# Kernel optimization log

Measured on AMD Instinct MI355X. Metric: run time of the kernel, lower is better.

## Reference

```python
import jax, jax.numpy as jnp
import numpy as np
from jax import lax

D_MODEL = 192
D_STATE = 16
D_CONV = 4
EXPAND = 2
D_INNER = D_MODEL * EXPAND           # 384
DT_RANK = (D_MODEL + 15) // 16       # 12
B, H, W = 4, 32, 32
N = H * W                            # 1024


def layernorm(x, g, b, eps=1e-5):
    m = x.mean(-1, keepdims=True)
    v = ((x - m) ** 2).mean(-1, keepdims=True)
    return (x - m) / jnp.sqrt(v + eps) * g + b


def mamba(u, Win, cw, cb, Wxp, Wdt, bdt, Alog, Dp, Wout):
    """mamba-ssm Mamba block. u: (B, L, d_model)."""
    Bb, L, _ = u.shape
    xz = u @ Win.T                                  # (B,L,2*d_inner)
    xh, z = jnp.split(xz, 2, axis=-1)
    # causal depthwise conv1d
    xc = xh.transpose(0, 2, 1)                      # (B,d_inner,L)
    xc = lax.conv_general_dilated(
        xc, cw[:, None, :], (1,), [(D_CONV - 1, 0)],
        feature_group_count=D_INNER,
        dimension_numbers=('NCH', 'OIH', 'NCH')) + cb[None, :, None]
    xs = jax.nn.silu(xc).transpose(0, 2, 1)         # (B,L,d_inner)
    dbl = xs @ Wxp.T                                # (B,L,dt_rank+2*d_state)
    dt = dbl[..., :DT_RANK]
    Bm = dbl[..., DT_RANK:DT_RANK + D_STATE]
    Cm = dbl[..., DT_RANK + D_STATE:]
    dt = jax.nn.softplus(dt @ Wdt.T + bdt)          # (B,L,d_inner)
    A = -jnp.exp(Alog)                              # (d_inner,d_state)

    def step(h, inp):
        dt_t, B_t, C_t, x_t = inp                   # (B,di),(B,ds),(B,ds),(B,di)
        dA = jnp.exp(dt_t[..., None] * A)           # (B,di,ds)
        h = dA * h + dt_t[..., None] * B_t[:, None, :] * x_t[..., None]
        return h, jnp.einsum('bds,bs->bd', h, C_t)

    h0 = jnp.zeros((Bb, D_INNER, D_STATE), u.dtype)
    _, ys = lax.scan(step, h0, (dt.transpose(1, 0, 2), Bm.transpose(1, 0, 2),
                                Cm.transpose(1, 0, 2), xs.transpose(1, 0, 2)))
    y = ys.transpose(1, 0, 2) + xs * Dp
    y = y * jax.nn.silu(z)
    return y @ Wout.T


mamba4 = jax.vmap(mamba)  # batched over the 4 scan directions


def to_col(x):    # row-major -> column-major sequence order
    return x.reshape(-1, H, W, D_MODEL).transpose(0, 2, 1, 3).reshape(-1, N, D_MODEL)


def from_col(x):  # inverse of to_col
    return x.reshape(-1, W, H, D_MODEL).transpose(0, 2, 1, 3).reshape(-1, N, D_MODEL)


def setup_inputs() -> dict:
    key = jax.random.key(0)
    ks = iter(jax.random.split(key, 32))
    s = 0.02
    d, di, ds, r = D_MODEL, D_INNER, D_STATE, DT_RANK
    inp = {}
    inp['x'] = jax.random.normal(next(ks), (B, d, H, W), jnp.float32)
    inp['norm_g'] = jnp.ones((d,), jnp.float32)
    inp['norm_b'] = jnp.zeros((d,), jnp.float32)
    inp['in_w'] = jax.random.normal(next(ks), (d, d), jnp.float32) * s
    inp['in_b'] = jnp.zeros((d,), jnp.float32)
    # 4 stacked Mamba blocks
    inp['m_in_w'] = jax.random.normal(next(ks), (4, 2 * di, d), jnp.float32) * s
    inp['m_conv_w'] = jax.random.normal(next(ks), (4, di, D_CONV), jnp.float32) * s
    inp['m_conv_b'] = jnp.zeros((4, di), jnp.float32)
    inp['m_xp_w'] = jax.random.normal(next(ks), (4, r + 2 * ds, di), jnp.float32) * s
    inp['m_dt_w'] = jax.random.normal(next(ks), (4, di, r), jnp.float32) * s
    inp['m_dt_b'] = jax.random.normal(next(ks), (4, di), jnp.float32) * 0.1 - 4.0
    inp['m_Alog'] = jnp.log(jnp.tile(jnp.arange(1, ds + 1, dtype=jnp.float32), (4, di, 1)))
    inp['m_D'] = jnp.ones((4, di), jnp.float32)
    inp['m_out_w'] = jax.random.normal(next(ks), (4, d, di), jnp.float32) * s
    # fusion MLP
    inp['f_w1'] = jax.random.normal(next(ks), (2 * d, 4 * d), jnp.float32) * s
    inp['f_b1'] = jnp.zeros((2 * d,), jnp.float32)
    inp['f_w2'] = jax.random.normal(next(ks), (d, 2 * d), jnp.float32) * s
    inp['f_b2'] = jnp.zeros((d,), jnp.float32)
    inp['o_w'] = jax.random.normal(next(ks), (d, d), jnp.float32) * s
    inp['o_b'] = jnp.zeros((d,), jnp.float32)
    inp['on_g'] = jnp.ones((d,), jnp.float32)
    inp['on_b'] = jnp.zeros((d,), jnp.float32)
    return inp


def reference(x, norm_g, norm_b, in_w, in_b, m_in_w, m_conv_w, m_conv_b,
              m_xp_w, m_dt_w, m_dt_b, m_Alog, m_D, m_out_w,
              f_w1, f_b1, f_w2, f_b2, o_w, o_b, on_g, on_b):
    xs = x.reshape(B, D_MODEL, N).transpose(0, 2, 1)     # b c h w -> b (hw) c
    xs = layernorm(xs, norm_g, norm_b)
    xp = xs @ in_w.T + in_b
    col = to_col(xp)
    seqs = jnp.stack([xp, jnp.flip(xp, 1), col, jnp.flip(col, 1)], 0)  # (4,B,N,C)
    ys = mamba4(seqs, m_in_w, m_conv_w, m_conv_b, m_xp_w, m_dt_w, m_dt_b,
                m_Alog, m_D, m_out_w)
    o0 = ys[0]
    o1 = jnp.flip(ys[1], 1)
    o2 = from_col(ys[2])
    o3 = from_col(jnp.flip(ys[3], 1))
    fused = jnp.concatenate([o0, o1, o2, o3], -1)        # (B,N,4C)
    hdn = jax.nn.gelu(fused @ f_w1.T + f_b1, approximate=False)
    hdn = hdn @ f_w2.T + f_b2
    out = hdn @ o_w.T + o_b
    out = layernorm(out, on_g, on_b) + xs
    return out.transpose(0, 2, 1).reshape(B, D_MODEL, H, W)
```

## Files before the change

### kernel.cpp

```cpp
#include <hip/hip_runtime.h>
#include <cstddef>

#define DM 192
#define DI 384
#define DS 16
#define DR 12
#define L 1024
#define ROWS 4096
#define SEG 32
#define ST  32

typedef unsigned short ushortx;
typedef short bf16x8 __attribute__((ext_vector_type(8)));
typedef float f32x4  __attribute__((ext_vector_type(4)));

__device__ __forceinline__ float wave_sum(float v) {
  #pragma unroll
  for (int off = 32; off > 0; off >>= 1) v += __shfl_xor(v, off);
  return v;
}

__device__ __forceinline__ ushortx f2bf(float x) {
  unsigned u = __float_as_uint(x);
  u += 0x7fffu + ((u >> 16) & 1u);
  return (ushortx)(u >> 16);
}
__device__ __forceinline__ float bf2f(ushortx u) {
  return __uint_as_float(((unsigned)u) << 16);
}

__device__ __forceinline__ int map_row(int t, int mode) {
  switch (mode) {
    case 1: return 1023 - t;
    case 2: return ((t & 31) << 5) | (t >> 5);
    case 3: { int u = 1023 - t; return ((u & 31) << 5) | (u >> 5); }
    case 4: return 1023 - (((t & 31) << 5) | (t >> 5));
    default: return t;
  }
}

struct WcvtArgs {
  const float* src[7];
  unsigned int off[7];
  unsigned int n[7];
};
__global__ __launch_bounds__(256) void prep_kernel(
    WcvtArgs a, ushortx* __restrict__ dst,
    const float* __restrict__ x, const float* __restrict__ g,
    const float* __restrict__ b, float* __restrict__ xs, ushortx* __restrict__ xs_bf)
{
  if (blockIdx.y < 7) {
    int w = blockIdx.y;
    int i = (blockIdx.x * 256 + threadIdx.x) * 4;
    if (i < (int)a.n[w]) {
      float4 v = *(const float4*)(a.src[w] + i);
      ushort4 o;
      o.x = f2bf(v.x); o.y = f2bf(v.y); o.z = f2bf(v.z); o.w = f2bf(v.w);
      *(ushort4*)(dst + a.off[w] + i) = o;
    }
    return;
  }
  int wave = threadIdx.x >> 6;
  int lane = threadIdx.x & 63;
  int r = blockIdx.x * 4 + wave;
  int bb = r >> 10, n = r & 1023;
  const float* xb = x + (size_t)bb * DM * L + n;
  float v[3];
  float s = 0.f, s2 = 0.f;
  #pragma unroll
  for (int j = 0; j < 3; ++j) {
    int c = lane + j * 64;
    v[j] = xb[(size_t)c * L];
    s += v[j]; s2 += v[j] * v[j];
  }
  s = wave_sum(s); s2 = wave_sum(s2);
  float mean = s * (1.f / DM);
  float var  = s2 * (1.f / DM) - mean * mean;
  float rstd = rsqrtf(var + 1e-5f);
  float* xo = xs + (size_t)r * DM;
  ushortx* xob = xs_bf + (size_t)r * DM;
  #pragma unroll
  for (int j = 0; j < 3; ++j) {
    int c = lane + j * 64;
    float val = (v[j] - mean) * rstd * g[c] + b[c];
    xo[c] = val;
    xob[c] = f2bf(val);
  }
}

template <int BM, int BN>
__global__ __launch_bounds__(256) void gemm_kernel(
    const ushortx* __restrict__ A, int lda, const ushortx* __restrict__ W,
    const float* __restrict__ bias, float* __restrict__ C, ushortx* __restrict__ Cb,
    int N, int K, int ldc, int coff, int4 perm, int act,
    long astride, long wstride, long cstride, int coffstride)
{
  constexpr int MF = BM / 32;
  constexpr int NF = BN / 32;
  constexpr int AR = (BM * 32) / (256 * 8);
  constexpr int BR = (BN * 32) / (256 * 8);
  __shared__ __align__(16) short As[2][BM][40];
  __shared__ __align__(16) short Bs[2][BN][40];

  int z = blockIdx.z;
  A += (size_t)z * astride;
  W += (size_t)z * wstride;
  if (C)  C  += (size_t)z * cstride;
  if (Cb) Cb += (size_t)z * cstride;
  int permMode = (z == 0) ? perm.x : (z == 1) ? perm.y : (z == 2) ? perm.z : perm.w;
  int co = coff + z * coffstride;

  int tid = threadIdx.x;
  int m0 = blockIdx.x * BM;
  int n0 = blockIdx.y * BN;

  int ar, ak;
  if (AR == 2) { ar = tid >> 1; ak = (tid & 1) * 16; }
  else         { ar = tid >> 2; ak = (tid & 3) * 8; }
  int arow = m0 + ar;
  int amrow = (arow & ~1023) | map_row(arow & 1023, permMode);
  const ushortx* ap = A + (size_t)amrow * lda + ak;

  int bn, bk;
  if (BR == 2) { bn = tid >> 1; bk = (tid & 1) * 16; }
  else         { bn = tid >> 2; bk = (tid & 3) * 8; }
  const ushortx* wp = W + (size_t)(n0 + bn) * K + bk;
  bool bok = (n0 + bn) < N;

  int lane = tid & 63;
  int w = tid >> 6, wm = w >> 1, wn = w & 1;
  int lm = lane & 15, lq = lane >> 4;

  f32x4 acc[MF][NF];
  #pragma unroll
  for (int i = 0; i < MF; ++i)
    #pragma unroll
    for (int j = 0; j < NF; ++j) acc[i][j] = (f32x4){0.f, 0.f, 0.f, 0.f};

  const bf16x8 zz = {0, 0, 0, 0, 0, 0, 0, 0};
  bf16x8 ra[AR], rb[BR];

  #pragma unroll
  for (int u = 0; u < AR; ++u) ra[u] = *(const bf16x8*)(ap + u * 8);
  #pragma unroll
  for (int u = 0; u < BR; ++u) rb[u] = bok ? *(const bf16x8*)(wp + u * 8) : zz;
  #pragma unroll
  for (int u = 0; u < AR; ++u) *(bf16x8*)&As[0][ar][ak + u * 8] = ra[u];
  #pragma unroll
  for (int u = 0; u < BR; ++u) *(bf16x8*)&Bs[0][bn][bk + u * 8] = rb[u];
  __syncthreads();

  int niter = K >> 5;
  for (int ki = 0; ki < niter; ++ki) {
    int cur = ki & 1;
    if (ki + 1 < niter) {
      int k0 = (ki + 1) * 32;
      #pragma unroll
      for (int u = 0; u < AR; ++u) ra[u] = *(const bf16x8*)(ap + k0 + u * 8);
      #pragma unroll
      for (int u = 0; u < BR; ++u) rb[u] = bok ? *(const bf16x8*)(wp + k0 + u * 8) : zz;
    }
    bf16x8 fa[MF], fb[NF];
    #pragma unroll
    for (int i = 0; i < MF; ++i)
      fa[i] = *(const bf16x8*)&As[cur][wm * (BM / 2) + i * 16 + lm][lq * 8];
    #pragma unroll
    for (int j = 0; j < NF; ++j)
      fb[j] = *(const bf16x8*)&Bs[cur][wn * (BN / 2) + j * 16 + lm][lq * 8];
    #pragma unroll
    for (int i = 0; i < MF; ++i)
      #pragma unroll
      for (int j = 0; j < NF; ++j)
        acc[i][j] = __builtin_amdgcn_mfma_f32_16x16x32_bf16(fa[i], fb[j], acc[i][j], 0, 0, 0);
    if (ki + 1 < niter) {
      int nxt = cur ^ 1;
      #pragma unroll
      for (int u = 0; u < AR; ++u) *(bf16x8*)&As[nxt][ar][ak + u * 8] = ra[u];
      #pragma unroll
      for (int u = 0; u < BR; ++u) *(bf16x8*)&Bs[nxt][bn][bk + u * 8] = rb[u];
      __syncthreads();
    }
  }

  #pragma unroll
  for (int i = 0; i < MF; ++i) {
    #pragma unroll
    for (int r = 0; r < 4; ++r) {
      int row = m0 + wm * (BM / 2) + i * 16 + lq * 4 + r;
      #pragma unroll
      for (int j = 0; j < NF; ++j) {
        int n = n0 + wn * (BN / 2) + j * 16 + lm;
        if (n < N) {
          float v = acc[i][j][r];
          if (bias) v += bias[n];
          if (act == 1) v = 0.5f * v * (1.f + erff(v * 0.70710678118f));
          if (C)  C [(size_t)row * ldc + co + n] = v;
          if (Cb) Cb[(size_t)row * ldc + co + n] = f2bf(v);
        }
      }
    }
  }
}

__global__ __launch_bounds__(256) void gemm_ln_kernel(
    const ushortx* __restrict__ A, const ushortx* __restrict__ W,
    const float* __restrict__ ob, const float* __restrict__ g,
    const float* __restrict__ b, const float* __restrict__ xs,
    float* __restrict__ out)
{
  __shared__ __align__(16) char smem[64 * 200 * 4];
  short* As0 = (short*)smem;
  short* As1 = As0 + 64 * 40;
  short* Bs0 = As1 + 64 * 40;
  short* Bs1 = Bs0 + 192 * 40;
  float* Ct  = (float*)smem;

  int tid = threadIdx.x;
  int m0 = blockIdx.x * 64;

  int ar = tid >> 2, ak = (tid & 3) * 8;
  const ushortx* ap = A + (size_t)(m0 + ar) * DM + ak;

  int lane = tid & 63;
  int w = tid >> 6, wm = w >> 1, wn = w & 1;
  int lm = lane & 15, lq = lane >> 4;

  f32x4 acc[2][6];
  #pragma unroll
  for (int i = 0; i < 2; ++i)
    #pragma unroll
    for (int j = 0; j < 6; ++j) acc[i][j] = (f32x4){0.f, 0.f, 0.f, 0.f};

  bf16x8 ra, rb[3];
  ra = *(const bf16x8*)ap;
  #pragma unroll
  for (int u = 0; u < 3; ++u) {
    int c = tid + u * 256;
    rb[u] = *(const bf16x8*)(W + (size_t)(c >> 2) * DM + (c & 3) * 8);
  }
  *(bf16x8*)&As0[ar * 40 + ak] = ra;
  #pragma unroll
  for (int u = 0; u < 3; ++u) {
    int c = tid + u * 256;
    *(bf16x8*)&Bs0[(c >> 2) * 40 + (c & 3) * 8] = rb[u];
  }
  __syncthreads();

  const int niter = DM / 32;
  for (int ki = 0; ki < niter; ++ki) {
    short* Ac = (ki & 1) ? As1 : As0;
    short* Bc = (ki & 1) ? Bs1 : Bs0;
    if (ki + 1 < niter) {
      int k0 = (ki + 1) * 32;
      ra = *(const bf16x8*)(ap + k0);
      #pragma unroll
      for (int u = 0; u < 3; ++u) {
        int c = tid + u * 256;
        rb[u] = *(const bf16x8*)(W + (size_t)(c >> 2) * DM + (c & 3) * 8 + k0);
      }
    }
    bf16x8 fa[2], fb[6];
    #pragma unroll
    for (int i = 0; i < 2; ++i)
      fa[i] = *(const bf16x8*)&Ac[(wm * 32 + i * 16 + lm) * 40 + lq * 8];
    #pragma unroll
    for (int j = 0; j < 6; ++j)
      fb[j] = *(const bf16x8*)&Bc[(wn * 96 + j * 16 + lm) * 40 + lq * 8];
    #pragma unroll
    for (int i = 0; i < 2; ++i)
      #pragma unroll
      for (int j = 0; j < 6; ++j)
        acc[i][j] = __builtin_amdgcn_mfma_f32_16x16x32_bf16(fa[i], fb[j], acc[i][j], 0, 0, 0);
    if (ki + 1 < niter) {
      short* An = (ki & 1) ? As0 : As1;
      short* Bn = (ki & 1) ? Bs0 : Bs1;
      *(bf16x8*)&An[ar * 40 + ak] = ra;
      #pragma unroll
      for (int u = 0; u < 3; ++u) {
        int c = tid + u * 256;
        *(bf16x8*)&Bn[(c >> 2) * 40 + (c & 3) * 8] = rb[u];
      }
    }
    __syncthreads();
  }

  #pragma unroll
  for (int i = 0; i < 2; ++i) {
    #pragma unroll
    for (int r = 0; r < 4; ++r) {
      int row = wm * 32 + i * 16 + lq * 4 + r;
      #pragma unroll
      for (int j = 0; j < 6; ++j) {
        int col = wn * 96 + j * 16 + lm;
        Ct[row * 200 + col] = acc[i][j][r] + ob[col];
      }
    }
  }
  __syncthreads();

  int row = tid >> 2, p = tid & 3;
  const float* base = Ct + row * 200 + p * 48;
  float s = 0.f, s2 = 0.f;
  #pragma unroll
  for (int c = 0; c < 48; ++c) { float v = base[c]; s += v; s2 += v * v; }
  s  += __shfl_xor(s, 1);  s  += __shfl_xor(s, 2);
  s2 += __shfl_xor(s2, 1); s2 += __shfl_xor(s2, 2);
  float mean = s * (1.f / DM);
  float var  = s2 * (1.f / DM) - mean * mean;
  float rstd = rsqrtf(var + 1e-5f);
  int gr = m0 + row, bb = gr >> 10, n = gr & 1023;
  const float* xsr = xs + (size_t)gr * DM + p * 48;
  float* op = out + (size_t)bb * DM * L + n;
  #pragma unroll
  for (int c48 = 0; c48 < 48; ++c48) {
    int c = p * 48 + c48;
    float val = (base[c48] - mean) * rstd * g[c] + b[c] + xsr[c48];
    op[(size_t)c * L] = val;
  }
}

__global__ __launch_bounds__(256) void conv_silu_kernel(
    const ushortx* __restrict__ xz, const float* __restrict__ cw,
    const float* __restrict__ cb, ushortx* __restrict__ xsm_bf)
{
  int idx = blockIdx.x * 256 + threadIdx.x;
  int d = idx % DI;
  int rest = idx / DI;
  int tq = rest & 255;
  int seq = rest >> 8;
  int k = seq >> 2;
  int t0 = tq * 4;
  const ushortx* xh = xz + (size_t)seq * L * (2 * DI) + d;
  const float* w = cw + ((size_t)k * DI + d) * 4;
  float w0 = w[0], w1 = w[1], w2 = w[2], w3 = w[3];
  float bias = cb[k * DI + d];
  float in[7];
  #pragma unroll
  for (int j = 0; j < 7; ++j) {
    int t = t0 - 3 + j;
    in[j] = (t >= 0) ? bf2f(xh[(size_t)t * (2 * DI)]) : 0.f;
  }
  ushortx* yo = xsm_bf + ((size_t)seq * L + t0) * DI + d;
  #pragma unroll
  for (int i = 0; i < 4; ++i) {
    float acc = bias;
    acc = fmaf(w0, in[i],     acc);
    acc = fmaf(w1, in[i + 1], acc);
    acc = fmaf(w2, in[i + 2], acc);
    acc = fmaf(w3, in[i + 3], acc);
    float sig = 1.f / (1.f + __expf(-acc));
    yo[(size_t)i * DI] = f2bf(acc * sig);
  }
}

__global__ __launch_bounds__(256) void dt_kernel(
    const float* __restrict__ dbl, const float* __restrict__ Wdt,
    const float* __restrict__ bdt, ushortx* __restrict__ dt)
{
  int idx = blockIdx.x * 256 + threadIdx.x;
  int d = idx % DI;
  int row = idx / DI;
  int k = row >> 12;
  const float* dl = dbl + (size_t)row * 44;
  const float* w = Wdt + ((size_t)k * DI + d) * DR;
  float acc = bdt[k * DI + d];
  #pragma unroll
  for (int r = 0; r < DR; ++r) acc = fmaf(w[r], dl[r], acc);
  float v = (acc > 20.f) ? acc : log1pf(__expf(acc));
  dt[idx] = f2bf(v);
}

__global__ __launch_bounds__(64) void scan_pass1(
    const float* __restrict__ dbl, const ushortx* __restrict__ dt,
    const ushortx* __restrict__ xsm_bf, const float* __restrict__ Alog,
    float* __restrict__ hseg, float* __restrict__ Sseg)
{
  __shared__ __align__(16) float sB[ST][16];
  int seq = blockIdx.y, g = blockIdx.z, k = seq >> 2;
  int d = blockIdx.x * 64 + threadIdx.x;

  const float* bbase = dbl + ((size_t)seq * L + g * ST) * 44 + 12;
  #pragma unroll
  for (int j = 0; j < 2; ++j) {
    int i = threadIdx.x + j * 64;
    int t = i >> 2, q = (i & 3) * 4;
    *(float4*)&sB[t][q] = *(const float4*)(bbase + (size_t)t * 44 + q);
  }
  float A[16];
  const float* alp = Alog + ((size_t)k * DI + d) * DS;
  #pragma unroll
  for (int s = 0; s < 16; ++s) A[s] = -__expf(alp[s]);

  const ushortx* dtp = dt     + ((size_t)seq * L + g * ST) * DI + d;
  const ushortx* xp  = xsm_bf + ((size_t)seq * L + g * ST) * DI + d;
  __syncthreads();

  float h[16];
  #pragma unroll
  for (int s = 0; s < 16; ++s) h[s] = 0.f;
  float sdt = 0.f;
  float rDt[4], rX[4];
  #pragma unroll
  for (int j = 0; j < 4; ++j) {
    rDt[j] = bf2f(dtp[(size_t)j * DI]);
    rX [j] = bf2f(xp [(size_t)j * DI]);
  }

  #pragma unroll 4
  for (int t = 0; t < ST; ++t) {
    float dtv = rDt[t & 3], xv = rX[t & 3];
    if (t + 4 < ST) {
      rDt[t & 3] = bf2f(dtp[(size_t)(t + 4) * DI]);
      rX [t & 3] = bf2f(xp [(size_t)(t + 4) * DI]);
    }
    float dtx = dtv * xv;
    sdt += dtv;
    #pragma unroll
    for (int s = 0; s < 16; ++s) {
      float dA = __expf(dtv * A[s]);
      h[s] = fmaf(dA, h[s], dtx * sB[t][s]);
    }
  }
  float* hp = hseg + (((size_t)seq * SEG + g) * DI + d) * DS;
  #pragma unroll
  for (int s = 0; s < 16; ++s) hp[s] = h[s];
  Sseg[((size_t)seq * SEG + g) * DI + d] = sdt;
}

__global__ __launch_bounds__(64) void scan_mid(
    float* __restrict__ hseg, const float* __restrict__ Sseg,
    const float* __restrict__ Alog)
{
  int seq = blockIdx.y, k = seq >> 2;
  int d = blockIdx.x * 64 + threadIdx.x;
  float A[16];
  const float* alp = Alog + ((size_t)k * DI + d) * DS;
  #pragma unroll
  for (int s = 0; s < 16; ++s) A[s] = -__expf(alp[s]);
  float h[16];
  #pragma unroll
  for (int s = 0; s < 16; ++s) h[s] = 0.f;
  for (int g = 0; g < SEG; ++g) {
    float* hp = hseg + (((size_t)seq * SEG + g) * DI + d) * DS;
    float Sg = Sseg[((size_t)seq * SEG + g) * DI + d];
    float tmp[16];
    #pragma unroll
    for (int s = 0; s < 16; ++s) tmp[s] = hp[s];
    #pragma unroll
    for (int s = 0; s < 16; ++s) hp[s] = h[s];
    #pragma unroll
    for (int s = 0; s < 16; ++s)
      h[s] = fmaf(h[s], __expf(A[s] * Sg), tmp[s]);
  }
}

__global__ __launch_bounds__(64) void scan_pass2(
    const float* __restrict__ dbl, const ushortx* __restrict__ dt,
    const ushortx* __restrict__ xz,
    ushortx* __restrict__ xy,
    const float* __restrict__ Alog, const float* __restrict__ Dp,
    const float* __restrict__ hseg)
{
  __shared__ __align__(16) float sBC[ST][32];
  int seq = blockIdx.y, g = blockIdx.z, k = seq >> 2;
  int d = blockIdx.x * 64 + threadIdx.x;

  const float* bcbase = dbl + ((size_t)seq * L + g * ST) * 44 + 12;
  #pragma unroll
  for (int j = 0; j < 4; ++j) {
    int i = threadIdx.x + j * 64;
    int t = i >> 3, q = (i & 7) * 4;
    *(float4*)&sBC[t][q] = *(const float4*)(bcbase + (size_t)t * 44 + q);
  }
  float A[16];
  const float* alp = Alog + ((size_t)k * DI + d) * DS;
  #pragma unroll
  for (int s = 0; s < 16; ++s) A[s] = -__expf(alp[s]);
  float Dv = Dp[k * DI + d];

  float h[16];
  {
    const float* hp = hseg + (((size_t)seq * SEG + g) * DI + d) * DS;
    #pragma unroll
    for (int s = 0; s < 16; ++s) h[s] = hp[s];
  }

  const ushortx* dtp = dt + ((size_t)seq * L + g * ST) * DI + d;
  const ushortx* zp  = xz + ((size_t)seq * L + g * ST) * (2 * DI) + DI + d;
  ushortx*       yp  = xy + ((size_t)seq * L + g * ST) * DI + d;
  __syncthreads();

  float rDt[4], rX[4], rZ[4];
  #pragma unroll
  for (int j = 0; j < 4; ++j) {
    rDt[j] = bf2f(dtp[(size_t)j * DI]);
    rX [j] = bf2f(yp [(size_t)j * DI]);
    rZ [j] = bf2f(zp [(size_t)j * (2 * DI)]);
  }

  #pragma unroll 4
  for (int t = 0; t < ST; ++t) {
    float dtv = rDt[t & 3], xv = rX[t & 3], zv = rZ[t & 3];
    if (t + 4 < ST) {
      rDt[t & 3] = bf2f(dtp[(size_t)(t + 4) * DI]);
      rX [t & 3] = bf2f(yp [(size_t)(t + 4) * DI]);
      rZ [t & 3] = bf2f(zp [(size_t)(t + 4) * (2 * DI)]);
    }
    float dtx = dtv * xv;
    float y = 0.f;
    #pragma unroll
    for (int s = 0; s < 16; ++s) {
      float dA = __expf(dtv * A[s]);
      h[s] = fmaf(dA, h[s], dtx * sBC[t][s]);
      y = fmaf(h[s], sBC[t][16 + s], y);
    }
    y = fmaf(Dv, xv, y);
    float sig = 1.f / (1.f + __expf(-zv));
    yp[(size_t)t * DI] = f2bf(y * (zv * sig));
  }
}

template <int BM, int BN>
static inline void gemm(const ushortx* A, int lda, const ushortx* W, const float* bias,
                        float* C, ushortx* Cb,
                        int N, int K, int ldc, int coff, int4 perm, int act,
                        int nz, long astride, long wstride, long cstride, int coffstride,
                        hipStream_t s) {
  dim3 grid(ROWS / BM, (N + BN - 1) / BN, nz);
  gemm_kernel<BM, BN><<<grid, 256, 0, s>>>(A, lda, W, bias, C, Cb, N, K, ldc, coff, perm, act,
                                           astride, wstride, cstride, coffstride);
}

extern "C" void kernel_launch(void* const* d_in, const int* in_sizes, int n_in,
                              void* d_out, int out_size, void* d_ws, size_t ws_size,
                              hipStream_t stream) {
  (void)in_sizes; (void)n_in; (void)out_size; (void)ws_size;
  const float* x        = (const float*)d_in[0];
  const float* norm_g   = (const float*)d_in[1];
  const float* norm_b   = (const float*)d_in[2];
  const float* in_w     = (const float*)d_in[3];
  const float* in_b     = (const float*)d_in[4];
  const float* m_in_w   = (const float*)d_in[5];
  const float* m_conv_w = (const float*)d_in[6];
  const float* m_conv_b = (const float*)d_in[7];
  const float* m_xp_w   = (const float*)d_in[8];
  const float* m_dt_w   = (const float*)d_in[9];
  const float* m_dt_b   = (const float*)d_in[10];
  const float* m_Alog   = (const float*)d_in[11];
  const float* m_D      = (const float*)d_in[12];
  const float* m_out_w  = (const float*)d_in[13];
  const float* f_w1     = (const float*)d_in[14];
  const float* f_b1     = (const float*)d_in[15];
  const float* f_w2     = (const float*)d_in[16];
  const float* f_b2     = (const float*)d_in[17];
  const float* o_w      = (const float*)d_in[18];
  const float* o_b      = (const float*)d_in[19];
  const float* on_g     = (const float*)d_in[20];
  const float* on_b     = (const float*)d_in[21];
  float* out = (float*)d_out;

  float* ws   = (float*)d_ws;
  float* xs   = ws;
  float* dbl  = xs + 786432;
  float* hseg = dbl + 720896;
  float* Sseg = hseg + 3145728;
  ushortx* xs_bf  = (ushortx*)(Sseg + 196608);
  ushortx* xp_bf  = xs_bf + 786432;
  ushortx* wbf    = xp_bf + 786432;
  ushortx* dt_bf  = wbf + 1394688;
  ushortx* xz_bf  = dt_bf + 6291456;
  ushortx* xsm_bf = xz_bf + 12582912;
  ushortx* fused_bf = xz_bf;
  ushortx* hdn_bf   = fused_bf + 3145728;
  ushortx* h2_bf    = hdn_bf + 1572864;

  const unsigned W_IN = 0, W_MIN = 36864, W_XP = 626688, W_OUT = 694272,
                 W_F1 = 989184, W_F2 = 1284096, W_O = 1357824;

  int4 p0 = make_int4(0, 0, 0, 0);
  int4 pfwd = make_int4(0, 1, 2, 3);
  int4 pinv = make_int4(0, 1, 2, 4);

  {
    WcvtArgs a;
    a.src[0] = in_w;    a.off[0] = W_IN;  a.n[0] = 36864;
    a.src[1] = m_in_w;  a.off[1] = W_MIN; a.n[1] = 589824;
    a.src[2] = m_xp_w;  a.off[2] = W_XP;  a.n[2] = 67584;
    a.src[3] = m_out_w; a.off[3] = W_OUT; a.n[3] = 294912;
    a.src[4] = f_w1;    a.off[4] = W_F1;  a.n[4] = 294912;
    a.src[5] = f_w2;    a.off[5] = W_F2;  a.n[5] = 73728;
    a.src[6] = o_w;     a.off[6] = W_O;   a.n[6] = 36864;
    prep_kernel<<<dim3(1024, 8), 256, 0, stream>>>(a, wbf, x, norm_g, norm_b, xs, xs_bf);
  }
  gemm<64, 64>(xs_bf, DM, wbf + W_IN, in_b, nullptr, xp_bf, DM, DM, DM, 0, p0, 0,
               1, 0, 0, 0, 0, stream);
  gemm<128, 128>(xp_bf, DM, wbf + W_MIN, nullptr, nullptr, xz_bf, 2 * DI, DM, 2 * DI, 0, pfwd, 0,
                 4, 0, (long)2 * DI * DM, (long)ROWS * 2 * DI, 0, stream);
  conv_silu_kernel<<<(16 * 256 * DI) / 256, 256, 0, stream>>>(xz_bf, m_conv_w, m_conv_b, xsm_bf);
  gemm<64, 64>(xsm_bf, DI, wbf + W_XP, nullptr, dbl, nullptr, 44, DI, 44, 0, p0, 0,
               4, (long)ROWS * DI, (long)44 * DI, (long)ROWS * 44, 0, stream);
  dt_kernel<<<(16 * L * DI) / 256, 256, 0, stream>>>(dbl, m_dt_w, m_dt_b, dt_bf);
  scan_pass1<<<dim3(DI / 64, 16, SEG), 64, 0, stream>>>(dbl, dt_bf, xsm_bf, m_Alog, hseg, Sseg);
  scan_mid<<<dim3(DI / 64, 16), 64, 0, stream>>>(hseg, Sseg, m_Alog);
  scan_pass2<<<dim3(DI / 64, 16, SEG), 64, 0, stream>>>(dbl, dt_bf, xz_bf, xsm_bf,
                                                        m_Alog, m_D, hseg);
  gemm<64, 64>(xsm_bf, DI, wbf + W_OUT, nullptr, nullptr, fused_bf, DM, DI, 4 * DM, 0, pinv, 0,
               4, (long)ROWS * DI, (long)DM * DI, 0, DM, stream);
  gemm<64, 64>(fused_bf, 4 * DM, wbf + W_F1, f_b1, nullptr, hdn_bf, 2 * DM, 4 * DM, 2 * DM,
               0, p0, 1, 1, 0, 0, 0, 0, stream);
  gemm<64, 64>(hdn_bf, 2 * DM, wbf + W_F2, f_b2, nullptr, h2_bf, DM, 2 * DM, DM, 0, p0, 0,
               1, 0, 0, 0, 0, stream);
  gemm_ln_kernel<<<64, 256, 0, stream>>>(h2_bf, wbf + W_O, o_b, on_g, on_b, xs, out);
}
```

Before: 299.6 us.

## Fold out_proj into fuse-W1 and fuse-W2 into output projection via weight products

Precomputes combined weights on device: each direction's Mamba out_proj is multiplied into its slice of f_w1, and f_w2 is multiplied into o_w with a folded bias. The tail then becomes one K=1536 GEMM over the four scan outputs (with inverse row permutation and GELU) plus one K=384 GEMM fused with LayerNorm, replacing four kernels. This removes the fused and h2 intermediate tensors and two GEMM launches. In exchange it adds small per-call weight-product GEMMs and a longer-K GEMM, and rounding the combined weights to bf16 changes numerics slightly.

```diff
diff --git a/kernel.cpp b/kernel.cpp
--- a/kernel.cpp
+++ b/kernel.cpp
@@ -40,26 +40,56 @@
 }
 
 struct WcvtArgs {
-  const float* src[7];
-  unsigned int off[7];
-  unsigned int n[7];
+  const float* src[5];
+  unsigned int off[5];
+  unsigned int n[5];
 };
 __global__ __launch_bounds__(256) void prep_kernel(
     WcvtArgs a, ushortx* __restrict__ dst,
+    const float* __restrict__ ow, unsigned owt_off,
+    const float* __restrict__ fw2, unsigned f2t_off,
     const float* __restrict__ x, const float* __restrict__ g,
-    const float* __restrict__ b, float* __restrict__ xs, ushortx* __restrict__ xs_bf)
-{
-  if (blockIdx.y < 7) {
-    int w = blockIdx.y;
+    const float* __restrict__ b, float* __restrict__ xs, ushortx* __restrict__ xs_bf,
+    const float* __restrict__ o_w, const float* __restrict__ f_b2,
+    const float* __restrict__ o_b, float* __restrict__ o_b2)
+{
+  int y = blockIdx.y;
+  if (y < 5) {
     int i = (blockIdx.x * 256 + threadIdx.x) * 4;
-    if (i < (int)a.n[w]) {
-      float4 v = *(const float4*)(a.src[w] + i);
+    if (i < (int)a.n[y]) {
+      float4 v = *(const float4*)(a.src[y] + i);
       ushort4 o;
       o.x = f2bf(v.x); o.y = f2bf(v.y); o.z = f2bf(v.z); o.w = f2bf(v.w);
-      *(ushort4*)(dst + a.off[w] + i) = o;
+      *(ushort4*)(dst + a.off[y] + i) = o;
     }
     return;
   }
+  if (y == 5) {
+    int i = blockIdx.x * 256 + threadIdx.x;
+    if (i < 4 * 384 * 192) {
+      int j = i % 192, d = (i / 192) % 384, k = i / (192 * 384);
+      dst[owt_off + i] = f2bf(ow[(size_t)k * 73728 + (size_t)j * 384 + d]);
+    }
+    return;
+  }
+  if (y == 6) {
+    int i = blockIdx.x * 256 + threadIdx.x;
+    if (i < 384 * 192) {
+      int j = i % 192, dd = i / 192;
+      dst[f2t_off + i] = f2bf(fw2[(size_t)j * 384 + dd]);
+    }
+    return;
+  }
+  if (y == 8) {
+    if (blockIdx.x == 0 && threadIdx.x < DM) {
+      int n = threadIdx.x;
+      float acc = o_b[n];
+      for (int j = 0; j < DM; ++j) acc = fmaf(o_w[(size_t)n * DM + j], f_b2[j], acc);
+      o_b2[n] = acc;
+    }
+    return;
+  }
+  if (blockIdx.x >= 1024) return;
   int wave = threadIdx.x >> 6;
   int lane = threadIdx.x & 63;
   int r = blockIdx.x * 4 + wave;
@@ -202,6 +232,86 @@
   }
 }
 
+__global__ __launch_bounds__(256) void gemm_ksum_kernel(
+    const ushortx* __restrict__ Y, const ushortx* __restrict__ Wc,
+    const float* __restrict__ bias, ushortx* __restrict__ Cb, int4 perm)
+{
+  __shared__ __align__(16) short As[2][64][40];
+  __shared__ __align__(16) short Bs[2][64][40];
+  int tid = threadIdx.x;
+  int m0 = blockIdx.x * 64;
+  int n0 = blockIdx.y * 64;
+  int ar = tid >> 2, ak = (tid & 3) * 8;
+  int bn = tid >> 2, bk = (tid & 3) * 8;
+  const ushortx* wp = Wc + (size_t)(n0 + bn) * 1536 + bk;
+
+  int lane = tid & 63;
+  int w = tid >> 6, wm = w >> 1, wn = w & 1;
+  int lm = lane & 15, lq = lane >> 4;
+
+  f32x4 acc[2][2];
+  #pragma unroll
+  for (int i = 0; i < 2; ++i)
+    #pragma unroll
+    for (int j = 0; j < 2; ++j) acc[i][j] = (f32x4){0.f, 0.f, 0.f, 0.f};
+
+  int row = m0 + ar;
+  auto aload = [&](int ki) -> bf16x8 {
+    int dir = ki / 12;
+    int kk = (ki - dir * 12) * 32;
+    int mode = (dir == 0) ? perm.x : (dir == 1) ? perm.y : (dir == 2) ? perm.z : perm.w;
+    int mrow = (row & ~1023) | map_row(row & 1023, mode);
+    return *(const bf16x8*)(Y + (size_t)dir * ROWS * DI + (size_t)mrow * DI + kk + ak);
+  };
+
+  bf16x8 ra = aload(0);
+  bf16x8 rb = *(const bf16x8*)wp;
+  *(bf16x8*)&As[0][ar][ak] = ra;
+  *(bf16x8*)&Bs[0][bn][bk] = rb;
+  __syncthreads();
+
+  for (int ki = 0; ki < 48; ++ki) {
+    int cur = ki & 1;
+    if (ki + 1 < 48) {
+      ra = aload(ki + 1);
+      rb = *(const bf16x8*)(wp + (ki + 1) * 32);
+    }
+    bf16x8 fa[2], fb[2];
+    #pragma unroll
+    for (int i = 0; i < 2; ++i)
+      fa[i] = *(const bf16x8*)&As[cur][wm * 32 + i * 16 + lm][lq * 8];
+    #pragma unroll
+    for (int j = 0; j < 2; ++j)
+      fb[j] = *(const bf16x8*)&Bs[cur][wn * 32 + j * 16 + lm][lq * 8];
+    #pragma unroll
+    for (int i = 0; i < 2; ++i)
+      #pragma unroll
+      for (int j = 0; j < 2; ++j)
+        acc[i][j] = __builtin_amdgcn_mfma_f32_16x16x32_bf16(fa[i], fb[j], acc[i][j], 0, 0, 0);
+    if (ki + 1 < 48) {
+      int nxt = cur ^ 1;
+      *(bf16x8*)&As[nxt][ar][ak] = ra;
+      *(bf16x8*)&Bs[nxt][bn][bk] = rb;
+      __syncthreads();
+    }
+  }
+
+  #pragma unroll
+  for (int i = 0; i < 2; ++i) {
+    #pragma unroll
+    for (int r = 0; r < 4; ++r) {
+      int orow = m0 + wm * 32 + i * 16 + lq * 4 + r;
+      #pragma unroll
+      for (int j = 0; j < 2; ++j) {
+        int n = n0 + wn * 32 + j * 16 + lm;
+        float v = acc[i][j][r] + bias[n];
+        v = 0.5f * v * (1.f + erff(v * 0.70710678118f));
+        Cb[(size_t)orow * 384 + n] = f2bf(v);
+      }
+    }
+  }
+}
+
 __global__ __launch_bounds__(256) void gemm_ln_kernel(
     const ushortx* __restrict__ A, const ushortx* __restrict__ W,
     const float* __restrict__ ob, const float* __restrict__ g,
@@ -219,7 +329,7 @@
   int m0 = blockIdx.x * 64;
 
   int ar = tid >> 2, ak = (tid & 3) * 8;
-  const ushortx* ap = A + (size_t)(m0 + ar) * DM + ak;
+  const ushortx* ap = A + (size_t)(m0 + ar) * 384 + ak;
 
   int lane = tid & 63;
   int w = tid >> 6, wm = w >> 1, wn = w & 1;
@@ -236,7 +346,7 @@
   #pragma unroll
   for (int u = 0; u < 3; ++u) {
     int c = tid + u * 256;
-    rb[u] = *(const bf16x8*)(W + (size_t)(c >> 2) * DM + (c & 3) * 8);
+    rb[u] = *(const bf16x8*)(W + (size_t)(c >> 2) * 384 + (c & 3) * 8);
   }
   *(bf16x8*)&As0[ar * 40 + ak] = ra;
   #pragma unroll
@@ -246,7 +356,7 @@
   }
   __syncthreads();
 
-  const int niter = DM / 32;
+  const int niter = 384 / 32;
   for (int ki = 0; ki < niter; ++ki) {
     short* Ac = (ki & 1) ? As1 : As0;
     short* Bc = (ki & 1) ? Bs1 : Bs0;
@@ -256,7 +366,7 @@
       #pragma unroll
       for (int u = 0; u < 3; ++u) {
         int c = tid + u * 256;
-        rb[u] = *(const bf16x8*)(W + (size_t)(c >> 2) * DM + (c & 3) * 8 + k0);
+        rb[u] = *(const bf16x8*)(W + (size_t)(c >> 2) * 384 + (c & 3) * 8 + k0);
       }
     }
     bf16x8 fa[2], fb[6];
@@ -525,8 +635,8 @@
                         float* C, ushortx* Cb,
                         int N, int K, int ldc, int coff, int4 perm, int act,
                         int nz, long astride, long wstride, long cstride, int coffstride,
-                        hipStream_t s) {
-  dim3 grid(ROWS / BM, (N + BN - 1) / BN, nz);
+                        hipStream_t s, int M = ROWS) {
+  dim3 grid(M / BM, (N + BN - 1) / BN, nz);
   gemm_kernel<BM, BN><<<grid, 256, 0, s>>>(A, lda, W, bias, C, Cb, N, K, ldc, coff, perm, act,
                                            astride, wstride, cstride, coffstride);
 }
@@ -564,18 +674,19 @@
   float* dbl  = xs + 786432;
   float* hseg = dbl + 720896;
   float* Sseg = hseg + 3145728;
-  ushortx* xs_bf  = (ushortx*)(Sseg + 196608);
+  float* o_b2 = Sseg + 196608;
+  ushortx* xs_bf  = (ushortx*)(o_b2 + 256);
   ushortx* xp_bf  = xs_bf + 786432;
   ushortx* wbf    = xp_bf + 786432;
   ushortx* dt_bf  = wbf + 1394688;
   ushortx* xz_bf  = dt_bf + 6291456;
   ushortx* xsm_bf = xz_bf + 12582912;
-  ushortx* fused_bf = xz_bf;
-  ushortx* hdn_bf   = fused_bf + 3145728;
-  ushortx* h2_bf    = hdn_bf + 1572864;
-
-  const unsigned W_IN = 0, W_MIN = 36864, W_XP = 626688, W_OUT = 694272,
-                 W_F1 = 989184, W_F2 = 1284096, W_O = 1357824;
+  ushortx* Wc     = xsm_bf + 6291456;
+  ushortx* Wc2    = Wc + 589824;
+  ushortx* hdn_bf = xz_bf;
+
+  const unsigned W_IN = 0, W_MIN = 36864, W_XP = 626688, W_F1 = 694272,
+                 W_O = 989184, W_OWT = 1026048, W_F2T = 1320960;
 
   int4 p0 = make_int4(0, 0, 0, 0);
   int4 pfwd = make_int4(0, 1, 2, 3);
@@ -586,12 +697,16 @@
     a.src[0] = in_w;    a.off[0] = W_IN;  a.n[0] = 36864;
     a.src[1] = m_in_w;  a.off[1] = W_MIN; a.n[1] = 589824;
     a.src[2] = m_xp_w;  a.off[2] = W_XP;  a.n[2] = 67584;
-    a.src[3] = m_out_w; a.off[3] = W_OUT; a.n[3] = 294912;
-    a.src[4] = f_w1;    a.off[4] = W_F1;  a.n[4] = 294912;
-    a.src[5] = f_w2;    a.off[5] = W_F2;  a.n[5] = 73728;
-    a.src[6] = o_w;     a.off[6] = W_O;   a.n[6] = 36864;
-    prep_kernel<<<dim3(1024, 8), 256, 0, stream>>>(a, wbf, x, norm_g, norm_b, xs, xs_bf);
-  }
+    a.src[3] = f_w1;    a.off[3] = W_F1;  a.n[3] = 294912;
+    a.src[4] = o_w;     a.off[4] = W_O;   a.n[4] = 36864;
+    prep_kernel<<<dim3(1152, 9), 256, 0, stream>>>(
+        a, wbf, m_out_w, W_OWT, f_w2, W_F2T,
+        x, norm_g, norm_b, xs, xs_bf, o_w, f_b2, o_b, o_b2);
+  }
+  gemm<64, 64>(wbf + W_F1, 768, wbf + W_OWT, nullptr, nullptr, Wc,
+               384, 192, 1536, 0, p0, 0, 4, 192, 73728, 0, 384, stream, 384);
+  gemm<64, 64>(wbf + W_O, 192, wbf + W_F2T, nullptr, nullptr, Wc2,
+               384, 192, 384, 0, p0, 0, 1, 0, 0, 0, 0, stream, 192);
   gemm<64, 64>(xs_bf, DM, wbf + W_IN, in_b, nullptr, xp_bf, DM, DM, DM, 0, p0, 0,
                1, 0, 0, 0, 0, stream);
   gemm<128, 128>(xp_bf, DM, wbf + W_MIN, nullptr, nullptr, xz_bf, 2 * DI, DM, 2 * DI, 0, pfwd, 0,
@@ -604,11 +719,6 @@
   scan_mid<<<dim3(DI / 64, 16), 64, 0, stream>>>(hseg, Sseg, m_Alog);
   scan_pass2<<<dim3(DI / 64, 16, SEG), 64, 0, stream>>>(dbl, dt_bf, xz_bf, xsm_bf,
                                                         m_Alog, m_D, hseg);
-  gemm<64, 64>(xsm_bf, DI, wbf + W_OUT, nullptr, nullptr, fused_bf, DM, DI, 4 * DM, 0, pinv, 0,
-               4, (long)ROWS * DI, (long)DM * DI, 0, DM, stream);
-  gemm<64, 64>(fused_bf, 4 * DM, wbf + W_F1, f_b1, nullptr, hdn_bf, 2 * DM, 4 * DM, 2 * DM,
-               0, p0, 1, 1, 0, 0, 0, 0, stream);
-  gemm<64, 64>(hdn_bf, 2 * DM, wbf + W_F2, f_b2, nullptr, h2_bf, DM, 2 * DM, DM, 0, p0, 0,
-               1, 0, 0, 0, 0, stream);
-  gemm_ln_kernel<<<64, 256, 0, stream>>>(h2_bf, wbf + W_O, o_b, on_g, on_b, xs, out);
-}
+  gemm_ksum_kernel<<<dim3(ROWS / 64, 6), 256, 0, stream>>>(xsm_bf, Wc, f_b1, hdn_bf, pinv);
+  gemm_ln_kernel<<<64, 256, 0, stream>>>(hdn_bf, Wc2, o_b2, on_g, on_b, xs, out);
+}
```

After: 304.0 us. No clear change (+1.5%).

## Fold in_proj into mamba in_proj weights and fuse x_proj GEMM with dt projection

Applied to the files above, without the earlier changes.

The input projection weight and bias are folded into each direction's Mamba in_proj: a small GEMM computes the combined weight (m_in_w · in_w) and prep computes the combined bias. This removes the separate xp GEMM and its intermediate buffer, so the xz GEMM reads the layer-normed activations directly. The x_proj GEMM is also fused with the dt projection and softplus through a shared-memory tile, which drops the standalone dt_kernel and its re-read of dbl. In exchange there is an extra weight-product GEMM each call, bf16 rounding of the composed weights, and less parallelism in the fused dt epilogue (64 blocks per direction, each thread looping over 96 channels).

```diff
diff --git a/kernel.cpp b/kernel.cpp
--- a/kernel.cpp
+++ b/kernel.cpp
@@ -40,26 +40,48 @@
 }
 
 struct WcvtArgs {
-  const float* src[7];
-  unsigned int off[7];
-  unsigned int n[7];
+  const float* src[6];
+  unsigned int off[6];
+  unsigned int n[6];
 };
 __global__ __launch_bounds__(256) void prep_kernel(
     WcvtArgs a, ushortx* __restrict__ dst,
+    const float* __restrict__ in_w, unsigned int_off,
+    const float* __restrict__ in_b, float* __restrict__ bC,
     const float* __restrict__ x, const float* __restrict__ g,
     const float* __restrict__ b, float* __restrict__ xs, ushortx* __restrict__ xs_bf)
 {
-  if (blockIdx.y < 7) {
-    int w = blockIdx.y;
+  int y = blockIdx.y;
+  if (y < 6) {
     int i = (blockIdx.x * 256 + threadIdx.x) * 4;
-    if (i < (int)a.n[w]) {
-      float4 v = *(const float4*)(a.src[w] + i);
+    if (i < (int)a.n[y]) {
+      float4 v = *(const float4*)(a.src[y] + i);
       ushort4 o;
       o.x = f2bf(v.x); o.y = f2bf(v.y); o.z = f2bf(v.z); o.w = f2bf(v.w);
-      *(ushort4*)(dst + a.off[w] + i) = o;
+      *(ushort4*)(dst + a.off[y] + i) = o;
     }
     return;
   }
+  if (y == 6) {
+    int i = blockIdx.x * 256 + threadIdx.x;
+    if (i < DM * DM) {
+      int n = i / DM, j = i % DM;
+      dst[int_off + i] = f2bf(in_w[(size_t)j * DM + n]);
+    }
+    return;
+  }
+  if (y == 8) {
+    int idx = blockIdx.x * 256 + threadIdx.x;
+    if (idx < 4 * 768) {
+      int k = idx / 768, n = idx % 768;
+      const float* wr = a.src[0] + (size_t)k * 768 * DM + (size_t)n * DM;
+      float acc = 0.f;
+      for (int j = 0; j < DM; ++j) acc = fmaf(wr[j], in_b[j], acc);
+      bC[idx] = acc;
+    }
+    return;
+  }
+  if (blockIdx.x >= 1024) return;
   int wave = threadIdx.x >> 6;
   int lane = threadIdx.x & 63;
   int r = blockIdx.x * 4 + wave;
@@ -93,7 +115,7 @@
     const ushortx* __restrict__ A, int lda, const ushortx* __restrict__ W,
     const float* __restrict__ bias, float* __restrict__ C, ushortx* __restrict__ Cb,
     int N, int K, int ldc, int coff, int4 perm, int act,
-    long astride, long wstride, long cstride, int coffstride)
+    long astride, long wstride, long cstride, int coffstride, int bstride)
 {
   constexpr int MF = BM / 32;
   constexpr int NF = BN / 32;
@@ -107,6 +129,7 @@
   W += (size_t)z * wstride;
   if (C)  C  += (size_t)z * cstride;
   if (Cb) Cb += (size_t)z * cstride;
+  if (bias) bias += (size_t)z * bstride;
   int permMode = (z == 0) ? perm.x : (z == 1) ? perm.y : (z == 2) ? perm.z : perm.w;
   int co = coff + z * coffstride;
 
@@ -199,6 +222,114 @@
         }
       }
     }
+  }
+}
+
+__global__ __launch_bounds__(256) void gemm_dbl_dt_kernel(
+    const ushortx* __restrict__ A, const ushortx* __restrict__ W,
+    float* __restrict__ dbl, const float* __restrict__ Wdt,
+    const float* __restrict__ bdt, ushortx* __restrict__ dt_bf)
+{
+  __shared__ __align__(16) short As[2][64][40];
+  __shared__ __align__(16) short Bs[2][64][40];
+  __shared__ float sW[DI * DR];
+  __shared__ float sb[DI];
+  __shared__ float Ct[64][46];
+
+  int z = blockIdx.z;
+  A += (size_t)z * ((size_t)ROWS * DI);
+  W += (size_t)z * (44 * DI);
+  const float* wdt = Wdt + (size_t)z * DI * DR;
+  const float* bd  = bdt + (size_t)z * DI;
+
+  int tid = threadIdx.x;
+  int m0 = blockIdx.x * 64;
+
+  for (int i = tid; i < (DI * DR) / 4; i += 256)
+    *(float4*)&sW[i * 4] = *(const float4*)(wdt + i * 4);
+  for (int i = tid; i < DI; i += 256) sb[i] = bd[i];
+
+  int ar = tid >> 2, ak = (tid & 3) * 8;
+  const ushortx* ap = A + (size_t)(m0 + ar) * DI + ak;
+  int bn = tid >> 2, bk = (tid & 3) * 8;
+  const ushortx* wp = W + (size_t)bn * DI + bk;
+  bool bok = bn < 44;
+
+  int lane = tid & 63;
+  int w = tid >> 6, wm = w >> 1, wn = w & 1;
+  int lm = lane & 15, lq = lane >> 4;
+
+  f32x4 acc[2][2];
+  #pragma unroll
+  for (int i = 0; i < 2; ++i)
+    #pragma unroll
+    for (int j = 0; j < 2; ++j) acc[i][j] = (f32x4){0.f, 0.f, 0.f, 0.f};
+
+  const bf16x8 zz = {0, 0, 0, 0, 0, 0, 0, 0};
+  bf16x8 ra = *(const bf16x8*)ap;
+  bf16x8 rb = bok ? *(const bf16x8*)wp : zz;
+  *(bf16x8*)&As[0][ar][ak] = ra;
+  *(bf16x8*)&Bs[0][bn][bk] = rb;
+  __syncthreads();
+
+  const int niter = DI / 32;
+  for (int ki = 0; ki < niter; ++ki) {
+    int cur = ki & 1;
+    if (ki + 1 < niter) {
+      int k0 = (ki + 1) * 32;
+      ra = *(const bf16x8*)(ap + k0);
+      rb = bok ? *(const bf16x8*)(wp + k0) : zz;
+    }
+    bf16x8 fa[2], fb[2];
+    #pragma unroll
+    for (int i = 0; i < 2; ++i)
+      fa[i] = *(const bf16x8*)&As[cur][wm * 32 + i * 16 + lm][lq * 8];
+    #pragma unroll
+    for (int j = 0; j < 2; ++j)
+      fb[j] = *(const bf16x8*)&Bs[cur][wn * 32 + j * 16 + lm][lq * 8];
+    #pragma unroll
+    for (int i = 0; i < 2; ++i)
+      #pragma unroll
+      for (int j = 0; j < 2; ++j)
+        acc[i][j] = __builtin_amdgcn_mfma_f32_16x16x32_bf16(fa[i], fb[j], acc[i][j], 0, 0, 0);
+    if (ki + 1 < niter) {
+      int nxt = cur ^ 1;
+      *(bf16x8*)&As[nxt][ar][ak] = ra;
+      *(bf16x8*)&Bs[nxt][bn][bk] = rb;
+      __syncthreads();
+    }
+  }
+
+  #pragma unroll
+  for (int i = 0; i < 2; ++i) {
+    #pragma unroll
+    for (int r = 0; r < 4; ++r) {
+      int row = wm * 32 + i * 16 + lq * 4 + r;
+      #pragma unroll
+      for (int j = 0; j < 2; ++j) {
+        int n = wn * 32 + j * 16 + lm;
+        if (n < 44) {
+          float v = acc[i][j][r];
+          Ct[row][n] = v;
+          dbl[((size_t)z * ROWS + m0 + row) * 44 + n] = v;
+        }
+      }
+    }
+  }
+  __syncthreads();
+
+  int row2 = tid >> 2, p = tid & 3;
+  float dl[DR];
+  #pragma unroll
+  for (int q = 0; q < DR; ++q) dl[q] = Ct[row2][q];
+  size_t gbase = ((size_t)z * ROWS + m0 + row2) * (size_t)DI;
+  for (int c = 0; c < 96; ++c) {
+    int ch = p + 4 * c;
+    float a2 = sb[ch];
+    #pragma unroll
+    for (int q = 0; q < DR; ++q) a2 = fmaf(sW[ch * DR + q], dl[q], a2);
+    float v = (a2 > 20.f) ? a2 : log1pf(__expf(a2));
+    dt_bf[gbase + ch] = f2bf(v);
   }
 }
 
@@ -353,23 +484,6 @@
   }
 }
 
-__global__ __launch_bounds__(256) void dt_kernel(
-    const float* __restrict__ dbl, const float* __restrict__ Wdt,
-    const float* __restrict__ bdt, ushortx* __restrict__ dt)
-{
-  int idx = blockIdx.x * 256 + threadIdx.x;
-  int d = idx % DI;
-  int row = idx / DI;
-  int k = row >> 12;
-  const float* dl = dbl + (size_t)row * 44;
-  const float* w = Wdt + ((size_t)k * DI + d) * DR;
-  float acc = bdt[k * DI + d];
-  #pragma unroll
-  for (int r = 0; r < DR; ++r) acc = fmaf(w[r], dl[r], acc);
-  float v = (acc > 20.f) ? acc : log1pf(__expf(acc));
-  dt[idx] = f2bf(v);
-}
-
 __global__ __launch_bounds__(64) void scan_pass1(
     const float* __restrict__ dbl, const ushortx* __restrict__ dt,
     const ushortx* __restrict__ xsm_bf, const float* __restrict__ Alog,
@@ -525,10 +639,10 @@
                         float* C, ushortx* Cb,
                         int N, int K, int ldc, int coff, int4 perm, int act,
                         int nz, long astride, long wstride, long cstride, int coffstride,
-                        hipStream_t s) {
-  dim3 grid(ROWS / BM, (N + BN - 1) / BN, nz);
+                        hipStream_t s, int M = ROWS, int bstride = 0) {
+  dim3 grid(M / BM, (N + BN - 1) / BN, nz);
   gemm_kernel<BM, BN><<<grid, 256, 0, s>>>(A, lda, W, bias, C, Cb, N, K, ldc, coff, perm, act,
-                                           astride, wstride, cstride, coffstride);
+                                           astride, wstride, cstride, coffstride, bstride);
 }
 
 extern "C" void kernel_launch(void* const* d_in, const int* in_sizes, int n_in,
@@ -564,18 +678,19 @@
   float* dbl  = xs + 786432;
   float* hseg = dbl + 720896;
   float* Sseg = hseg + 3145728;
-  ushortx* xs_bf  = (ushortx*)(Sseg + 196608);
-  ushortx* xp_bf  = xs_bf + 786432;
-  ushortx* wbf    = xp_bf + 786432;
-  ushortx* dt_bf  = wbf + 1394688;
+  float* bC   = Sseg + 196608;
+  ushortx* xs_bf  = (ushortx*)(bC + 4096);
+  ushortx* wbf    = xs_bf + 786432;
+  ushortx* WinC   = wbf + 1394688;
+  ushortx* dt_bf  = WinC + 589824;
   ushortx* xz_bf  = dt_bf + 6291456;
   ushortx* xsm_bf = xz_bf + 12582912;
   ushortx* fused_bf = xz_bf;
   ushortx* hdn_bf   = fused_bf + 3145728;
   ushortx* h2_bf    = hdn_bf + 1572864;
 
-  const unsigned W_IN = 0, W_MIN = 36864, W_XP = 626688, W_OUT = 694272,
-                 W_F1 = 989184, W_F2 = 1284096, W_O = 1357824;
+  const unsigned W_MIN = 0, W_XP = 589824, W_OUT = 657408, W_F1 = 952320,
+                 W_F2 = 1247232, W_O = 1320960, W_INT = 1357824;
 
   int4 p0 = make_int4(0, 0, 0, 0);
   int4 pfwd = make_int4(0, 1, 2, 3);
@@ -583,23 +698,23 @@
 
   {
     WcvtArgs a;
-    a.src[0] = in_w;    a.off[0] = W_IN;  a.n[0] = 36864;
-    a.src[1] = m_in_w;  a.off[1] = W_MIN; a.n[1] = 589824;
-    a.src[2] = m_xp_w;  a.off[2] = W_XP;  a.n[2] = 67584;
-    a.src[3] = m_out_w; a.off[3] = W_OUT; a.n[3] = 294912;
-    a.src[4] = f_w1;    a.off[4] = W_F1;  a.n[4] = 294912;
-    a.src[5] = f_w2;    a.off[5] = W_F2;  a.n[5] = 73728;
-    a.src[6] = o_w;     a.off[6] = W_O;   a.n[6] = 36864;
-    prep_kernel<<<dim3(1024, 8), 256, 0, stream>>>(a, wbf, x, norm_g, norm_b, xs, xs_bf);
-  }
-  gemm<64, 64>(xs_bf, DM, wbf + W_IN, in_b, nullptr, xp_bf, DM, DM, DM, 0, p0, 0,
-               1, 0, 0, 0, 0, stream);
-  gemm<128, 128>(xp_bf, DM, wbf + W_MIN, nullptr, nullptr, xz_bf, 2 * DI, DM, 2 * DI, 0, pfwd, 0,
-                 4, 0, (long)2 * DI * DM, (long)ROWS * 2 * DI, 0, stream);
+    a.src[0] = m_in_w;  a.off[0] = W_MIN; a.n[0] = 589824;
+    a.src[1] = m_xp_w;  a.off[1] = W_XP;  a.n[1] = 67584;
+    a.src[2] = m_out_w; a.off[2] = W_OUT; a.n[2] = 294912;
+    a.src[3] = f_w1;    a.off[3] = W_F1;  a.n[3] = 294912;
+    a.src[4] = f_w2;    a.off[4] = W_F2;  a.n[4] = 73728;
+    a.src[5] = o_w;     a.off[5] = W_O;   a.n[5] = 36864;
+    prep_kernel<<<dim3(1024, 9), 256, 0, stream>>>(
+        a, wbf, in_w, W_INT, in_b, bC, x, norm_g, norm_b, xs, xs_bf);
+  }
+  gemm<64, 64>(wbf + W_MIN, DM, wbf + W_INT, nullptr, nullptr, WinC,
+               DM, DM, DM, 0, p0, 0, 4, (long)768 * DM, 0, (long)768 * DM, 0,
+               stream, 768);
+  gemm<128, 128>(xs_bf, DM, WinC, bC, nullptr, xz_bf, 2 * DI, DM, 2 * DI, 0, pfwd, 0,
+                 4, 0, (long)768 * DM, (long)ROWS * 2 * DI, 0, stream, ROWS, 768);
   conv_silu_kernel<<<(16 * 256 * DI) / 256, 256, 0, stream>>>(xz_bf, m_conv_w, m_conv_b, xsm_bf);
-  gemm<64, 64>(xsm_bf, DI, wbf + W_XP, nullptr, dbl, nullptr, 44, DI, 44, 0, p0, 0,
-               4, (long)ROWS * DI, (long)44 * DI, (long)ROWS * 44, 0, stream);
-  dt_kernel<<<(16 * L * DI) / 256, 256, 0, stream>>>(dbl, m_dt_w, m_dt_b, dt_bf);
+  gemm_dbl_dt_kernel<<<dim3(ROWS / 64, 1, 4), 256, 0, stream>>>(
+      xsm_bf, wbf + W_XP, dbl, m_dt_w, m_dt_b, dt_bf);
   scan_pass1<<<dim3(DI / 64, 16, SEG), 64, 0, stream>>>(dbl, dt_bf, xsm_bf, m_Alog, hseg, Sseg);
   scan_mid<<<dim3(DI / 64, 16), 64, 0, stream>>>(hseg, Sseg, m_Alog);
   scan_pass2<<<dim3(DI / 64, 16, SEG), 64, 0, stream>>>(dbl, dt_bf, xz_bf, xsm_bf,
```

New measurement: 318.4 us. +6.3%, slower.

## Fold input projection into mamba in_proj weights via precomputed combined matrix

Applied to the files above, without the earlier changes.

Precomputes combined weights WinC = m_in_w @ in_w (per direction) and a combined bias m_in_w @ in_b, so the in_proj GEMM reads the layernormed activations directly instead of first materialising the in_w projection. This removes one GEMM pass over the activations and the xp buffer. In exchange it adds a small weight-weight GEMM and a serial bias dot-product kernel slice each call, and changes bf16 rounding since the product is rounded once instead of twice.

```diff
diff --git a/kernel.cpp b/kernel.cpp
--- a/kernel.cpp
+++ b/kernel.cpp
@@ -40,26 +40,48 @@
 }
 
 struct WcvtArgs {
-  const float* src[7];
-  unsigned int off[7];
-  unsigned int n[7];
+  const float* src[6];
+  unsigned int off[6];
+  unsigned int n[6];
 };
 __global__ __launch_bounds__(256) void prep_kernel(
     WcvtArgs a, ushortx* __restrict__ dst,
+    const float* __restrict__ in_w, unsigned int_off,
+    const float* __restrict__ in_b, float* __restrict__ bC,
     const float* __restrict__ x, const float* __restrict__ g,
     const float* __restrict__ b, float* __restrict__ xs, ushortx* __restrict__ xs_bf)
 {
-  if (blockIdx.y < 7) {
-    int w = blockIdx.y;
+  int y = blockIdx.y;
+  if (y < 6) {
     int i = (blockIdx.x * 256 + threadIdx.x) * 4;
-    if (i < (int)a.n[w]) {
-      float4 v = *(const float4*)(a.src[w] + i);
+    if (i < (int)a.n[y]) {
+      float4 v = *(const float4*)(a.src[y] + i);
       ushort4 o;
       o.x = f2bf(v.x); o.y = f2bf(v.y); o.z = f2bf(v.z); o.w = f2bf(v.w);
-      *(ushort4*)(dst + a.off[w] + i) = o;
+      *(ushort4*)(dst + a.off[y] + i) = o;
     }
     return;
   }
+  if (y == 6) {
+    int i = blockIdx.x * 256 + threadIdx.x;
+    if (i < DM * DM) {
+      int n = i / DM, j = i % DM;
+      dst[int_off + i] = f2bf(in_w[(size_t)j * DM + n]);
+    }
+    return;
+  }
+  if (y == 8) {
+    int idx = blockIdx.x * 256 + threadIdx.x;
+    if (idx < 4 * 768) {
+      int k = idx / 768, n = idx % 768;
+      const float* wr = a.src[0] + (size_t)k * 768 * DM + (size_t)n * DM;
+      float acc = 0.f;
+      for (int j = 0; j < DM; ++j) acc = fmaf(wr[j], in_b[j], acc);
+      bC[idx] = acc;
+    }
+    return;
+  }
+  if (blockIdx.x >= 1024) return;
   int wave = threadIdx.x >> 6;
   int lane = threadIdx.x & 63;
   int r = blockIdx.x * 4 + wave;
@@ -93,7 +115,7 @@
     const ushortx* __restrict__ A, int lda, const ushortx* __restrict__ W,
     const float* __restrict__ bias, float* __restrict__ C, ushortx* __restrict__ Cb,
     int N, int K, int ldc, int coff, int4 perm, int act,
-    long astride, long wstride, long cstride, int coffstride)
+    long astride, long wstride, long cstride, int coffstride, int bstride)
 {
   constexpr int MF = BM / 32;
   constexpr int NF = BN / 32;
@@ -107,6 +129,7 @@
   W += (size_t)z * wstride;
   if (C)  C  += (size_t)z * cstride;
   if (Cb) Cb += (size_t)z * cstride;
+  if (bias) bias += (size_t)z * bstride;
   int permMode = (z == 0) ? perm.x : (z == 1) ? perm.y : (z == 2) ? perm.z : perm.w;
   int co = coff + z * coffstride;
 
@@ -525,10 +548,10 @@
                         float* C, ushortx* Cb,
                         int N, int K, int ldc, int coff, int4 perm, int act,
                         int nz, long astride, long wstride, long cstride, int coffstride,
-                        hipStream_t s) {
-  dim3 grid(ROWS / BM, (N + BN - 1) / BN, nz);
+                        hipStream_t s, int M = ROWS, int bstride = 0) {
+  dim3 grid(M / BM, (N + BN - 1) / BN, nz);
   gemm_kernel<BM, BN><<<grid, 256, 0, s>>>(A, lda, W, bias, C, Cb, N, K, ldc, coff, perm, act,
-                                           astride, wstride, cstride, coffstride);
+                                           astride, wstride, cstride, coffstride, bstride);
 }
 
 extern "C" void kernel_launch(void* const* d_in, const int* in_sizes, int n_in,
@@ -564,18 +587,19 @@
   float* dbl  = xs + 786432;
   float* hseg = dbl + 720896;
   float* Sseg = hseg + 3145728;
-  ushortx* xs_bf  = (ushortx*)(Sseg + 196608);
-  ushortx* xp_bf  = xs_bf + 786432;
-  ushortx* wbf    = xp_bf + 786432;
-  ushortx* dt_bf  = wbf + 1394688;
+  float* bC   = Sseg + 196608;
+  ushortx* xs_bf  = (ushortx*)(bC + 4096);
+  ushortx* wbf    = xs_bf + 786432;
+  ushortx* WinC   = wbf + 1394688;
+  ushortx* dt_bf  = WinC + 589824;
   ushortx* xz_bf  = dt_bf + 6291456;
   ushortx* xsm_bf = xz_bf + 12582912;
   ushortx* fused_bf = xz_bf;
   ushortx* hdn_bf   = fused_bf + 3145728;
   ushortx* h2_bf    = hdn_bf + 1572864;
 
-  const unsigned W_IN = 0, W_MIN = 36864, W_XP = 626688, W_OUT = 694272,
-                 W_F1 = 989184, W_F2 = 1284096, W_O = 1357824;
+  const unsigned W_MIN = 0, W_XP = 589824, W_OUT = 657408, W_F1 = 952320,
+                 W_F2 = 1247232, W_O = 1320960, W_INT = 1357824;
 
   int4 p0 = make_int4(0, 0, 0, 0);
   int4 pfwd = make_int4(0, 1, 2, 3);
@@ -583,19 +607,20 @@
 
   {
     WcvtArgs a;
-    a.src[0] = in_w;    a.off[0] = W_IN;  a.n[0] = 36864;
-    a.src[1] = m_in_w;  a.off[1] = W_MIN; a.n[1] = 589824;
-    a.src[2] = m_xp_w;  a.off[2] = W_XP;  a.n[2] = 67584;
-    a.src[3] = m_out_w; a.off[3] = W_OUT; a.n[3] = 294912;
-    a.src[4] = f_w1;    a.off[4] = W_F1;  a.n[4] = 294912;
-    a.src[5] = f_w2;    a.off[5] = W_F2;  a.n[5] = 73728;
-    a.src[6] = o_w;     a.off[6] = W_O;   a.n[6] = 36864;
-    prep_kernel<<<dim3(1024, 8), 256, 0, stream>>>(a, wbf, x, norm_g, norm_b, xs, xs_bf);
-  }
-  gemm<64, 64>(xs_bf, DM, wbf + W_IN, in_b, nullptr, xp_bf, DM, DM, DM, 0, p0, 0,
-               1, 0, 0, 0, 0, stream);
-  gemm<128, 128>(xp_bf, DM, wbf + W_MIN, nullptr, nullptr, xz_bf, 2 * DI, DM, 2 * DI, 0, pfwd, 0,
-                 4, 0, (long)2 * DI * DM, (long)ROWS * 2 * DI, 0, stream);
+    a.src[0] = m_in_w;  a.off[0] = W_MIN; a.n[0] = 589824;
+    a.src[1] = m_xp_w;  a.off[1] = W_XP;  a.n[1] = 67584;
+    a.src[2] = m_out_w; a.off[2] = W_OUT; a.n[2] = 294912;
+    a.src[3] = f_w1;    a.off[3] = W_F1;  a.n[3] = 294912;
+    a.src[4] = f_w2;    a.off[4] = W_F2;  a.n[4] = 73728;
+    a.src[5] = o_w;     a.off[5] = W_O;   a.n[5] = 36864;
+    prep_kernel<<<dim3(1024, 9), 256, 0, stream>>>(
+        a, wbf, in_w, W_INT, in_b, bC, x, norm_g, norm_b, xs, xs_bf);
+  }
+  gemm<64, 64>(wbf + W_MIN, DM, wbf + W_INT, nullptr, nullptr, WinC,
+               DM, DM, DM, 0, p0, 0, 4, (long)768 * DM, 0, (long)768 * DM, 0,
+               stream, 768);
+  gemm<128, 128>(xs_bf, DM, WinC, bC, nullptr, xz_bf, 2 * DI, DM, 2 * DI, 0, pfwd, 0,
+                 4, 0, (long)768 * DM, (long)ROWS * 2 * DI, 0, stream, ROWS, 768);
   conv_silu_kernel<<<(16 * 256 * DI) / 256, 256, 0, stream>>>(xz_bf, m_conv_w, m_conv_b, xsm_bf);
   gemm<64, 64>(xsm_bf, DI, wbf + W_XP, nullptr, dbl, nullptr, 44, DI, 44, 0, p0, 0,
                4, (long)ROWS * DI, (long)44 * DI, (long)ROWS * 44, 0, stream);
```

Measured after the change: 308.9 us. 1.03x slower.
